# Kernel optimization log

Measured on AMD Instinct MI355X. Metric: run time of the kernel, lower is better.

Reference implementation:

```python
import jax, jax.numpy as jnp
import numpy as np

N_NODES = 50000


def gcn_conv(x, edge_index, W, b, n_nodes):
    # Linear transform first (as in PyG GCNConv), then normalized aggregation
    xw = x @ W  # [N, out]
    src, dst = edge_index[0], edge_index[1]
    loops = jnp.arange(n_nodes, dtype=src.dtype)
    s = jnp.concatenate([src, loops])  # add self-loops
    d = jnp.concatenate([dst, loops])
    deg = jax.ops.segment_sum(jnp.ones_like(s, dtype=xw.dtype), d, num_segments=n_nodes)
    dinv = jnp.where(deg > 0, jax.lax.rsqrt(deg), 0.0)
    norm = dinv[s] * dinv[d]  # [E+N]
    msg = xw[s] * norm[:, None]  # gather + scale
    out = jax.ops.segment_sum(msg, d, num_segments=n_nodes)  # scatter-add
    return out + b


def setup_inputs() -> dict:
    key = jax.random.key(0)
    k1, k2, k3, k4 = jax.random.split(key, 4)
    in_dim, hidden = 128, 128
    n_edges = 625000
    x = jax.random.normal(k1, (N_NODES, in_dim), dtype=jnp.float32)
    edge_index = jax.random.randint(k2, (2, n_edges), 0, N_NODES, dtype=jnp.int64)
    # glorot-ish scale
    W1 = jax.random.normal(k3, (in_dim, hidden), dtype=jnp.float32) * (1.0 / np.sqrt(in_dim))
    b1 = jnp.zeros((hidden,), dtype=jnp.float32)
    W2 = jax.random.normal(k4, (hidden, hidden), dtype=jnp.float32) * (1.0 / np.sqrt(hidden))
    b2 = jnp.zeros((hidden,), dtype=jnp.float32)
    return {"x": x, "edge_index": edge_index, "W1": W1, "b1": b1, "W2": W2, "b2": b2}


def reference(x, edge_index, W1, b1, W2, b2):
    n = x.shape[0]
    h = gcn_conv(x, edge_index, W1, b1, n)
    h = jax.nn.relu(h)
    # dropout(p=0.3) is identity in eval mode
    h = gcn_conv(h, edge_index, W2, b2, n)
    return jax.nn.relu(h)
```

## Files before the change

### kernel.cpp

```cpp
#include <hip/hip_runtime.h>
#include <hip/hip_bf16.h>

#define NNODES 50000
#define BKT 64
#define LP 136

typedef short bf16x8 __attribute__((ext_vector_type(8)));
typedef float f32x4 __attribute__((ext_vector_type(4)));

__device__ __forceinline__ unsigned short f2bf_rn(float f) {
    unsigned int u = __float_as_uint(f);
    return (unsigned short)((u + 0x7fffu + ((u >> 16) & 1u)) >> 16);
}
__device__ __forceinline__ float bf_lo(unsigned int u) { return __uint_as_float(u << 16); }
__device__ __forceinline__ float bf_hi(unsigned int u) { return __uint_as_float(u & 0xffff0000u); }


__global__ __launch_bounds__(256) void k_wt(const float* __restrict__ W1,
                                            const float* __restrict__ W2,
                                            unsigned short* __restrict__ WT1,
                                            unsigned short* __restrict__ WT2,
                                            int* __restrict__ cnt, int N) {
    __shared__ float tile[128 * 129];
    int b = blockIdx.x, t = threadIdx.x;
    if (b < 2) {
        const float* W = b ? W2 : W1;
        unsigned short* WT = b ? WT2 : WT1;
        for (int idx = t; idx < 128 * 128; idx += 256)
            tile[(idx >> 7) * 129 + (idx & 127)] = W[idx];
        __syncthreads();
        for (int idx = t; idx < 128 * 128; idx += 256) {
            int c = idx >> 7, k = idx & 127;
            WT[c * 128 + k] = f2bf_rn(tile[k * 129 + c]);
        }
    } else {
        int i = (b - 2) * 256 + t;
        if (i < N) cnt[i] = 0;
    }
}


__device__ __forceinline__ void gather_accum(const unsigned int* __restrict__ xwb,
                                             const int* __restrict__ cnt,
                                             const int* __restrict__ bp,
                                             int degc, int lane,
                                             float& ax, float& ay) {
    float px = 0.f, py = 0.f;
    int j = 0;
    for (; j + 8 <= degc; j += 8) {
        int4 q0 = *(const int4*)&bp[j];
        int4 q1 = *(const int4*)&bp[j + 4];
        unsigned int u0 = xwb[(size_t)q0.x * 64 + lane];
        unsigned int u1 = xwb[(size_t)q0.y * 64 + lane];
        unsigned int u2 = xwb[(size_t)q0.z * 64 + lane];
        unsigned int u3 = xwb[(size_t)q0.w * 64 + lane];
        unsigned int u4 = xwb[(size_t)q1.x * 64 + lane];
        unsigned int u5 = xwb[(size_t)q1.y * 64 + lane];
        unsigned int u6 = xwb[(size_t)q1.z * 64 + lane];
        unsigned int u7 = xwb[(size_t)q1.w * 64 + lane];
        float w0 = rsqrtf((float)cnt[q0.x] + 1.0f), w1 = rsqrtf((float)cnt[q0.y] + 1.0f);
        float w2 = rsqrtf((float)cnt[q0.z] + 1.0f), w3 = rsqrtf((float)cnt[q0.w] + 1.0f);
        float w4 = rsqrtf((float)cnt[q1.x] + 1.0f), w5 = rsqrtf((float)cnt[q1.y] + 1.0f);
        float w6 = rsqrtf((float)cnt[q1.z] + 1.0f), w7 = rsqrtf((float)cnt[q1.w] + 1.0f);
        ax = fmaf(bf_lo(u0), w0, ax);  ay = fmaf(bf_hi(u0), w0, ay);
        px = fmaf(bf_lo(u1), w1, px);  py = fmaf(bf_hi(u1), w1, py);
        ax = fmaf(bf_lo(u2), w2, ax);  ay = fmaf(bf_hi(u2), w2, ay);
        px = fmaf(bf_lo(u3), w3, px);  py = fmaf(bf_hi(u3), w3, py);
        ax = fmaf(bf_lo(u4), w4, ax);  ay = fmaf(bf_hi(u4), w4, ay);
        px = fmaf(bf_lo(u5), w5, px);  py = fmaf(bf_hi(u5), w5, py);
        ax = fmaf(bf_lo(u6), w6, ax);  ay = fmaf(bf_hi(u6), w6, ay);
        px = fmaf(bf_lo(u7), w7, px);  py = fmaf(bf_hi(u7), w7, py);
    }
    if (j + 4 <= degc) {
        int4 q = *(const int4*)&bp[j];
        unsigned int u0 = xwb[(size_t)q.x * 64 + lane];
        unsigned int u1 = xwb[(size_t)q.y * 64 + lane];
        unsigned int u2 = xwb[(size_t)q.z * 64 + lane];
        unsigned int u3 = xwb[(size_t)q.w * 64 + lane];
        float w0 = rsqrtf((float)cnt[q.x] + 1.0f), w1 = rsqrtf((float)cnt[q.y] + 1.0f);
        float w2 = rsqrtf((float)cnt[q.z] + 1.0f), w3 = rsqrtf((float)cnt[q.w] + 1.0f);
        ax = fmaf(bf_lo(u0), w0, ax);  ay = fmaf(bf_hi(u0), w0, ay);
        px = fmaf(bf_lo(u1), w1, px);  py = fmaf(bf_hi(u1), w1, py);
        ax = fmaf(bf_lo(u2), w2, ax);  ay = fmaf(bf_hi(u2), w2, ay);
        px = fmaf(bf_lo(u3), w3, px);  py = fmaf(bf_hi(u3), w3, py);
        j += 4;
    }
    for (; j < degc; ++j) {
        int s = bp[j];
        float wv = rsqrtf((float)cnt[s] + 1.0f);
        unsigned int u = xwb[(size_t)s * 64 + lane];
        ax = fmaf(bf_lo(u), wv, ax);
        ay = fmaf(bf_hi(u), wv, ay);
    }
    ax += px;
    ay += py;
}


__global__ __launch_bounds__(256) void k_gemmbucket(const float* __restrict__ X,
                                                    const unsigned short* __restrict__ WT,
                                                    unsigned short* __restrict__ Yb, int n,
                                                    const int* __restrict__ src,
                                                    const int* __restrict__ dst,
                                                    int* __restrict__ cnt,
                                                    int* __restrict__ bkt, int E, int EB) {
    __shared__ unsigned short Wl[128 * LP];
    int t = threadIdx.x;
    if ((int)blockIdx.x < EB) {
        int e = blockIdx.x * 256 + t;
        if (e < E) {
            int s = src[e], d = dst[e];
            int pos = atomicAdd(&cnt[d], 1);
            if (pos < BKT) bkt[(size_t)d * BKT + pos] = s;
        }
        return;
    }
    int gb = blockIdx.x - EB;
    int lane = t & 63, w = t >> 6;
    int m = lane & 15, quad = lane >> 4;
    int base = gb * 64 + w * 16;
    int row = min(base + m, n - 1);

    bf16x8 a[4];
#pragma unroll
    for (int kt = 0; kt < 4; ++kt) {
        const float* pa = &X[(size_t)row * 128 + kt * 32 + quad * 8];
        float4 v0 = *(const float4*)pa;
        float4 v1 = *(const float4*)(pa + 4);
        a[kt][0] = (short)f2bf_rn(v0.x); a[kt][1] = (short)f2bf_rn(v0.y);
        a[kt][2] = (short)f2bf_rn(v0.z); a[kt][3] = (short)f2bf_rn(v0.w);
        a[kt][4] = (short)f2bf_rn(v1.x); a[kt][5] = (short)f2bf_rn(v1.y);
        a[kt][6] = (short)f2bf_rn(v1.z); a[kt][7] = (short)f2bf_rn(v1.w);
    }
    for (int idx = t; idx < 128 * 16; idx += 256) {
        int r = idx >> 4, c8 = (idx & 15) << 3;
        *(uint4*)&Wl[r * LP + c8] = *(const uint4*)&WT[r * 128 + c8];
    }
    __syncthreads();

    f32x4 acc[8];
#pragma unroll
    for (int i = 0; i < 8; ++i) acc[i] = f32x4{0.f, 0.f, 0.f, 0.f};
#pragma unroll
    for (int kt = 0; kt < 4; ++kt) {
        int ko = kt * 32 + quad * 8;
#pragma unroll
        for (int ct = 0; ct < 8; ++ct) {
            bf16x8 b = *(const bf16x8*)&Wl[(ct * 16 + m) * LP + ko];
            acc[ct] = __builtin_amdgcn_mfma_f32_16x16x32_bf16(a[kt], b, acc[ct], 0, 0, 0);
        }
    }
    __syncthreads();

    unsigned short* ep = &Wl[w * 16 * LP];
#pragma unroll
    for (int ct = 0; ct < 8; ++ct)
#pragma unroll
        for (int r = 0; r < 4; ++r)
            ep[(quad * 4 + r) * LP + ct * 16 + m] = f2bf_rn(acc[ct][r]);
    __syncthreads();
    int rr = lane & 15, cc = lane >> 4;
    int orow = base + rr;
    if (orow < n) {
#pragma unroll
        for (int i2 = 0; i2 < 4; ++i2)
            ((uint4*)&Yb[(size_t)orow * 128])[cc * 4 + i2] =
                *(const uint4*)&ep[rr * LP + (cc * 4 + i2) * 8];
    }
}


__global__ __launch_bounds__(1024, 2) void k_aggemm(const unsigned int* __restrict__ xw1,
                                                    const int* __restrict__ cnt,
                                                    const int* __restrict__ bkt,
                                                    const float* __restrict__ bias,
                                                    const unsigned short* __restrict__ WT2,
                                                    unsigned short* __restrict__ xw2, int n) {
    __shared__ unsigned short Wl[128 * LP];
    __shared__ unsigned short At[16 * LP];
    int t = threadIdx.x, lane = t & 63, w = t >> 6;
    int base = blockIdx.x * 16;

    for (int idx = t; idx < 128 * 16; idx += 1024) {
        int r = idx >> 4, c8 = (idx & 15) << 3;
        *(uint4*)&Wl[r * LP + c8] = *(const uint4*)&WT2[r * 128 + c8];
    }

    int i = min(base + w, n - 1);
    int deg = cnt[i];
    int degc = min(deg, BKT);
    float di = rsqrtf((float)deg + 1.0f);
    unsigned int v0 = xw1[(size_t)i * 64 + lane];
    float ax = di * bf_lo(v0), ay = di * bf_hi(v0);
    gather_accum(xw1, cnt, &bkt[(size_t)i * BKT], degc, lane, ax, ay);
    float bx = bias[lane * 2], by = bias[lane * 2 + 1];
    ax = fmaxf(fmaf(di, ax, bx), 0.0f);
    ay = fmaxf(fmaf(di, ay, by), 0.0f);
    ((unsigned int*)&At[w * LP])[lane] = (unsigned)f2bf_rn(ax) | ((unsigned)f2bf_rn(ay) << 16);
    __syncthreads();

    int m = lane & 15, quad = lane >> 4;
    f32x4 acc = f32x4{0.f, 0.f, 0.f, 0.f};
    if (w < 8) {
        bf16x8 a[4];
#pragma unroll
        for (int kt = 0; kt < 4; ++kt)
            a[kt] = *(const bf16x8*)&At[m * LP + kt * 32 + quad * 8];
#pragma unroll
        for (int kt = 0; kt < 4; ++kt) {
            bf16x8 b = *(const bf16x8*)&Wl[(w * 16 + m) * LP + kt * 32 + quad * 8];
            acc = __builtin_amdgcn_mfma_f32_16x16x32_bf16(a[kt], b, acc, 0, 0, 0);
        }
    }
    __syncthreads();
    if (w < 8) {
#pragma unroll
        for (int r = 0; r < 4; ++r)
            At[(quad * 4 + r) * LP + w * 16 + m] = f2bf_rn(acc[r]);
    }
    __syncthreads();
    if (t < 256) {
        int row = t >> 4, q = t & 15;
        int orow = base + row;
        if (orow < n)
            *(uint4*)&xw2[(size_t)orow * 128 + q * 8] = *(const uint4*)&At[row * LP + q * 8];
    }
}


__global__ __launch_bounds__(256) void k_agg(const unsigned int* __restrict__ xwb,
                                             const int* __restrict__ cnt,
                                             const int* __restrict__ bkt,
                                             const float* __restrict__ bias,
                                             float* __restrict__ out, int n) {
    int lane = threadIdx.x & 63;
    int i = (blockIdx.x * 256 + threadIdx.x) >> 6;
    if (i >= n) return;
    int deg = cnt[i];
    int degc = min(deg, BKT);
    float di = rsqrtf((float)deg + 1.0f);
    unsigned int v0 = xwb[(size_t)i * 64 + lane];
    float ax = di * bf_lo(v0), ay = di * bf_hi(v0);
    gather_accum(xwb, cnt, &bkt[(size_t)i * BKT], degc, lane, ax, ay);
    float bx = bias[lane * 2], by = bias[lane * 2 + 1];
    ax = fmaxf(fmaf(di, ax, bx), 0.0f);
    ay = fmaxf(fmaf(di, ay, by), 0.0f);
    ((float2*)out)[(size_t)i * 64 + lane] = make_float2(ax, ay);
}


extern "C" void kernel_launch(void* const* d_in, const int* in_sizes, int n_in,
                              void* d_out, int out_size, void* d_ws, size_t ws_size,
                              hipStream_t stream) {
    const float* x  = (const float*)d_in[0];
    const int*   ei = (const int*)d_in[1];
    const float* W1 = (const float*)d_in[2];
    const float* b1 = (const float*)d_in[3];
    const float* W2 = (const float*)d_in[4];
    const float* b2 = (const float*)d_in[5];
    float* out = (float*)d_out;

    const int N = NNODES;
    const int E = in_sizes[1] / 2;
    const int* src = ei;
    const int* dst = ei + E;

    char* p = (char*)d_ws;
    size_t off = 0;
    auto take = [&](size_t bytes) -> void* {
        void* r = p + off;
        off = (off + bytes + 255) & ~(size_t)255;
        return r;
    };
    int* cnt = (int*)take((size_t)N * 4);
    int* bkt = (int*)take((size_t)N * BKT * 4);
    unsigned short* w1t = (unsigned short*)take(128 * 128 * 2);
    unsigned short* w2t = (unsigned short*)take(128 * 128 * 2);
    unsigned short* xw1 = (unsigned short*)take((size_t)N * 128 * 2);
    unsigned short* xw2 = (unsigned short*)take((size_t)N * 128 * 2);

    const int NB = (N + 255) / 256;
    const int EB = (E + 255) / 256;
    const int GB = (N + 63) / 64;

    k_wt<<<2 + NB, 256, 0, stream>>>(W1, W2, w1t, w2t, cnt, N);
    k_gemmbucket<<<EB + GB, 256, 0, stream>>>(x, w1t, xw1, N, src, dst, cnt, bkt, E, EB);
    k_aggemm<<<(N + 15) / 16, 1024, 0, stream>>>((const unsigned int*)xw1, cnt, bkt,
                                                 b1, w2t, xw2, N);
    k_agg<<<(N * 64 + 255) / 256, 256, 0, stream>>>((const unsigned int*)xw2, cnt, bkt,
                                                    b2, out, N);
}
```

Measured before the change: 205.0 us.

## Pack bucket indices as uint16, partition edge bucketing by XCD, read W from global

Neighbor bucket entries shrink from int32 to uint16, which halves bucket-table traffic on both write and gather. This relies on node ids staying below 65536. Edge bucketing now runs in 8 groups of blocks, each reading all edges with int4 dst loads and handling only destinations in its own node range, so atomics land on one XCD's L2 but dst is read 8 times. The GEMM part drops the LDS staging of W and its barriers and reads B fragments directly from global, using a smaller LDS buffer only for the epilogue.

```diff
diff --git a/kernel.cpp b/kernel.cpp
--- a/kernel.cpp
+++ b/kernel.cpp
@@ -4,6 +4,8 @@
 #define NNODES 50000
 #define BKT 64
 #define LP 136
+#define NXCD 8
+#define NPX 6250
 
 typedef short bf16x8 __attribute__((ext_vector_type(8)));
 typedef float f32x4 __attribute__((ext_vector_type(4)));
@@ -42,26 +44,29 @@
 
 __device__ __forceinline__ void gather_accum(const unsigned int* __restrict__ xwb,
                                              const int* __restrict__ cnt,
-                                             const int* __restrict__ bp,
+                                             const unsigned short* __restrict__ bp,
                                              int degc, int lane,
                                              float& ax, float& ay) {
     float px = 0.f, py = 0.f;
     int j = 0;
     for (; j + 8 <= degc; j += 8) {
-        int4 q0 = *(const int4*)&bp[j];
-        int4 q1 = *(const int4*)&bp[j + 4];
-        unsigned int u0 = xwb[(size_t)q0.x * 64 + lane];
-        unsigned int u1 = xwb[(size_t)q0.y * 64 + lane];
-        unsigned int u2 = xwb[(size_t)q0.z * 64 + lane];
-        unsigned int u3 = xwb[(size_t)q0.w * 64 + lane];
-        unsigned int u4 = xwb[(size_t)q1.x * 64 + lane];
-        unsigned int u5 = xwb[(size_t)q1.y * 64 + lane];
-        unsigned int u6 = xwb[(size_t)q1.z * 64 + lane];
-        unsigned int u7 = xwb[(size_t)q1.w * 64 + lane];
-        float w0 = rsqrtf((float)cnt[q0.x] + 1.0f), w1 = rsqrtf((float)cnt[q0.y] + 1.0f);
-        float w2 = rsqrtf((float)cnt[q0.z] + 1.0f), w3 = rsqrtf((float)cnt[q0.w] + 1.0f);
-        float w4 = rsqrtf((float)cnt[q1.x] + 1.0f), w5 = rsqrtf((float)cnt[q1.y] + 1.0f);
-        float w6 = rsqrtf((float)cnt[q1.z] + 1.0f), w7 = rsqrtf((float)cnt[q1.w] + 1.0f);
+        int4 q = *(const int4*)&bp[j];
+        int s0 = q.x & 0xffff, s1 = (int)((unsigned)q.x >> 16);
+        int s2 = q.y & 0xffff, s3 = (int)((unsigned)q.y >> 16);
+        int s4 = q.z & 0xffff, s5 = (int)((unsigned)q.z >> 16);
+        int s6 = q.w & 0xffff, s7 = (int)((unsigned)q.w >> 16);
+        unsigned int u0 = xwb[(size_t)s0 * 64 + lane];
+        unsigned int u1 = xwb[(size_t)s1 * 64 + lane];
+        unsigned int u2 = xwb[(size_t)s2 * 64 + lane];
+        unsigned int u3 = xwb[(size_t)s3 * 64 + lane];
+        unsigned int u4 = xwb[(size_t)s4 * 64 + lane];
+        unsigned int u5 = xwb[(size_t)s5 * 64 + lane];
+        unsigned int u6 = xwb[(size_t)s6 * 64 + lane];
+        unsigned int u7 = xwb[(size_t)s7 * 64 + lane];
+        float w0 = rsqrtf((float)cnt[s0] + 1.0f), w1 = rsqrtf((float)cnt[s1] + 1.0f);
+        float w2 = rsqrtf((float)cnt[s2] + 1.0f), w3 = rsqrtf((float)cnt[s3] + 1.0f);
+        float w4 = rsqrtf((float)cnt[s4] + 1.0f), w5 = rsqrtf((float)cnt[s5] + 1.0f);
+        float w6 = rsqrtf((float)cnt[s6] + 1.0f), w7 = rsqrtf((float)cnt[s7] + 1.0f);
         ax = fmaf(bf_lo(u0), w0, ax);  ay = fmaf(bf_hi(u0), w0, ay);
         px = fmaf(bf_lo(u1), w1, px);  py = fmaf(bf_hi(u1), w1, py);
         ax = fmaf(bf_lo(u2), w2, ax);  ay = fmaf(bf_hi(u2), w2, ay);
@@ -72,13 +77,15 @@
         px = fmaf(bf_lo(u7), w7, px);  py = fmaf(bf_hi(u7), w7, py);
     }
     if (j + 4 <= degc) {
-        int4 q = *(const int4*)&bp[j];
-        unsigned int u0 = xwb[(size_t)q.x * 64 + lane];
-        unsigned int u1 = xwb[(size_t)q.y * 64 + lane];
-        unsigned int u2 = xwb[(size_t)q.z * 64 + lane];
-        unsigned int u3 = xwb[(size_t)q.w * 64 + lane];
-        float w0 = rsqrtf((float)cnt[q.x] + 1.0f), w1 = rsqrtf((float)cnt[q.y] + 1.0f);
-        float w2 = rsqrtf((float)cnt[q.z] + 1.0f), w3 = rsqrtf((float)cnt[q.w] + 1.0f);
+        int2 q = *(const int2*)&bp[j];
+        int s0 = q.x & 0xffff, s1 = (int)((unsigned)q.x >> 16);
+        int s2 = q.y & 0xffff, s3 = (int)((unsigned)q.y >> 16);
+        unsigned int u0 = xwb[(size_t)s0 * 64 + lane];
+        unsigned int u1 = xwb[(size_t)s1 * 64 + lane];
+        unsigned int u2 = xwb[(size_t)s2 * 64 + lane];
+        unsigned int u3 = xwb[(size_t)s3 * 64 + lane];
+        float w0 = rsqrtf((float)cnt[s0] + 1.0f), w1 = rsqrtf((float)cnt[s1] + 1.0f);
+        float w2 = rsqrtf((float)cnt[s2] + 1.0f), w3 = rsqrtf((float)cnt[s3] + 1.0f);
         ax = fmaf(bf_lo(u0), w0, ax);  ay = fmaf(bf_hi(u0), w0, ay);
         px = fmaf(bf_lo(u1), w1, px);  py = fmaf(bf_hi(u1), w1, py);
         ax = fmaf(bf_lo(u2), w2, ax);  ay = fmaf(bf_hi(u2), w2, ay);
@@ -103,19 +110,47 @@
                                                     const int* __restrict__ src,
                                                     const int* __restrict__ dst,
                                                     int* __restrict__ cnt,
-                                                    int* __restrict__ bkt, int E, int EB) {
-    __shared__ unsigned short Wl[128 * LP];
+                                                    unsigned short* __restrict__ bkt,
+                                                    int E, int EBTOT) {
+    __shared__ unsigned short Ep[64 * LP];
     int t = threadIdx.x;
-    if ((int)blockIdx.x < EB) {
-        int e = blockIdx.x * 256 + t;
-        if (e < E) {
-            int s = src[e], d = dst[e];
-            int pos = atomicAdd(&cnt[d], 1);
-            if (pos < BKT) bkt[(size_t)d * BKT + pos] = s;
+    if ((int)blockIdx.x < EBTOT) {
+        int g = blockIdx.x & (NXCD - 1);
+        int kk = blockIdx.x >> 3;
+        int lo = g * NPX;
+        int SLOTS = E >> 2;
+        int idx = kk * 256 + t;
+        if (idx < SLOTS) {
+            int4 d4 = ((const int4*)dst)[idx];
+            int e0 = idx << 2;
+            if ((unsigned)(d4.x - lo) < (unsigned)NPX) {
+                int pos = atomicAdd(&cnt[d4.x], 1);
+                if (pos < BKT) bkt[(size_t)d4.x * BKT + pos] = (unsigned short)src[e0];
+            }
+            if ((unsigned)(d4.y - lo) < (unsigned)NPX) {
+                int pos = atomicAdd(&cnt[d4.y], 1);
+                if (pos < BKT) bkt[(size_t)d4.y * BKT + pos] = (unsigned short)src[e0 + 1];
+            }
+            if ((unsigned)(d4.z - lo) < (unsigned)NPX) {
+                int pos = atomicAdd(&cnt[d4.z], 1);
+                if (pos < BKT) bkt[(size_t)d4.z * BKT + pos] = (unsigned short)src[e0 + 2];
+            }
+            if ((unsigned)(d4.w - lo) < (unsigned)NPX) {
+                int pos = atomicAdd(&cnt[d4.w], 1);
+                if (pos < BKT) bkt[(size_t)d4.w * BKT + pos] = (unsigned short)src[e0 + 3];
+            }
+        }
+        if (kk == 0 && t < (E & 3)) {
+            int e = (E & ~3) + t;
+            int d = dst[e];
+            if ((unsigned)(d - lo) < (unsigned)NPX) {
+                int pos = atomicAdd(&cnt[d], 1);
+                if (pos < BKT) bkt[(size_t)d * BKT + pos] = (unsigned short)src[e];
+            }
         }
         return;
     }
-    int gb = blockIdx.x - EB;
+    int gb = blockIdx.x - EBTOT;
     int lane = t & 63, w = t >> 6;
     int m = lane & 15, quad = lane >> 4;
     int base = gb * 64 + w * 16;
@@ -132,11 +167,6 @@
         a[kt][4] = (short)f2bf_rn(v1.x); a[kt][5] = (short)f2bf_rn(v1.y);
         a[kt][6] = (short)f2bf_rn(v1.z); a[kt][7] = (short)f2bf_rn(v1.w);
     }
-    for (int idx = t; idx < 128 * 16; idx += 256) {
-        int r = idx >> 4, c8 = (idx & 15) << 3;
-        *(uint4*)&Wl[r * LP + c8] = *(const uint4*)&WT[r * 128 + c8];
-    }
-    __syncthreads();
 
     f32x4 acc[8];
 #pragma unroll
@@ -146,13 +176,12 @@
         int ko = kt * 32 + quad * 8;
 #pragma unroll
         for (int ct = 0; ct < 8; ++ct) {
-            bf16x8 b = *(const bf16x8*)&Wl[(ct * 16 + m) * LP + ko];
+            bf16x8 b = *(const bf16x8*)&WT[(ct * 16 + m) * 128 + ko];
             acc[ct] = __builtin_amdgcn_mfma_f32_16x16x32_bf16(a[kt], b, acc[ct], 0, 0, 0);
         }
     }
-    __syncthreads();
-
-    unsigned short* ep = &Wl[w * 16 * LP];
+
+    unsigned short* ep = &Ep[w * 16 * LP];
 #pragma unroll
     for (int ct = 0; ct < 8; ++ct)
 #pragma unroll
@@ -172,7 +201,7 @@
 
 __global__ __launch_bounds__(1024, 2) void k_aggemm(const unsigned int* __restrict__ xw1,
                                                     const int* __restrict__ cnt,
-                                                    const int* __restrict__ bkt,
+                                                    const unsigned short* __restrict__ bkt,
                                                     const float* __restrict__ bias,
                                                     const unsigned short* __restrict__ WT2,
                                                     unsigned short* __restrict__ xw2, int n) {
@@ -230,7 +259,7 @@
 
 __global__ __launch_bounds__(256) void k_agg(const unsigned int* __restrict__ xwb,
                                              const int* __restrict__ cnt,
-                                             const int* __restrict__ bkt,
+                                             const unsigned short* __restrict__ bkt,
                                              const float* __restrict__ bias,
                                              float* __restrict__ out, int n) {
     int lane = threadIdx.x & 63;
@@ -273,18 +302,20 @@
         return r;
     };
     int* cnt = (int*)take((size_t)N * 4);
-    int* bkt = (int*)take((size_t)N * BKT * 4);
+    unsigned short* bkt = (unsigned short*)take((size_t)N * BKT * 2);
     unsigned short* w1t = (unsigned short*)take(128 * 128 * 2);
     unsigned short* w2t = (unsigned short*)take(128 * 128 * 2);
     unsigned short* xw1 = (unsigned short*)take((size_t)N * 128 * 2);
     unsigned short* xw2 = (unsigned short*)take((size_t)N * 128 * 2);
 
     const int NB = (N + 255) / 256;
-    const int EB = (E + 255) / 256;
+    const int SLOTS = E / 4;
+    const int NBG = (SLOTS + 255) / 256;
+    const int EBTOT = NBG * NXCD;
     const int GB = (N + 63) / 64;
 
     k_wt<<<2 + NB, 256, 0, stream>>>(W1, W2, w1t, w2t, cnt, N);
-    k_gemmbucket<<<EB + GB, 256, 0, stream>>>(x, w1t, xw1, N, src, dst, cnt, bkt, E, EB);
+    k_gemmbucket<<<EBTOT + GB, 256, 0, stream>>>(x, w1t, xw1, N, src, dst, cnt, bkt, E, EBTOT);
     k_aggemm<<<(N + 15) / 16, 1024, 0, stream>>>((const unsigned int*)xw1, cnt, bkt,
                                                  b1, w2t, xw2, N);
     k_agg<<<(N * 64 + 255) / 256, 256, 0, stream>>>((const unsigned int*)xw2, cnt, bkt,
```

Result: slower. 209.9 us (+2.4%).
